# Kernel tuning notes

Hardware: AMD Instinct MI355X
Metric: run time of the kernel (lower is better)

Reference implementation:

```python
import jax, jax.numpy as jnp
import numpy as np

N_NODES = 50000
IN_F = 512
OUT_F = 512
N_EDGES = 1600000
DROP_P = 0.5
NEG_SLOPE = 0.01  # torch LeakyReLU default


def leaky_relu(x):
    return jnp.where(x >= 0, x, NEG_SLOPE * x)


def setup_inputs() -> dict:
    key = jax.random.key(0)
    k1, k2, k3, k4, k5, k6 = jax.random.split(key, 6)
    x = jax.random.normal(k1, (N_NODES, IN_F), dtype=jnp.float32)
    W = jax.random.normal(k2, (OUT_F, IN_F), dtype=jnp.float32) * (1.0 / np.sqrt(IN_F))
    # inverted dropout mask: bernoulli(keep)/keep, keep = 1 - p
    keep = 1.0 - DROP_P
    drop_mask = (jax.random.uniform(k3, (N_NODES, IN_F)) < keep).astype(jnp.float32) / keep
    adj_vals = jax.random.uniform(k4, (N_EDGES,), dtype=jnp.float32)
    adj_rows = jax.random.randint(k5, (N_EDGES,), 0, N_NODES, dtype=jnp.int32)
    adj_cols = jax.random.randint(k6, (N_EDGES,), 0, N_NODES, dtype=jnp.int32)
    return {"x": x, "W": W, "drop_mask": drop_mask, "adj_vals": adj_vals,
            "adj_rows": adj_rows, "adj_cols": adj_cols}


def reference(x, W, drop_mask, adj_vals, adj_rows, adj_cols):
    # support = Linear(dropout(x)); Linear weight is [out, in] (torch convention)
    support = jnp.einsum('ni,oi->no', x * drop_mask, W)  # [N, out]
    h = leaky_relu(support)
    # sparse adj @ h: out[r] += v * h[c]
    msgs = adj_vals[:, None] * h[adj_cols]               # [E, out]
    agg = jax.ops.segment_sum(msgs, adj_rows, num_segments=N_NODES)
    return leaky_relu(agg)
```

## Files before the change

### kernel.cpp

```cpp
#include <hip/hip_runtime.h>

#define NROWS 50000
#define NFEAT 512
#define NEDGE 1600000
#define SLOPE 0.01f

typedef unsigned short u16;
typedef __attribute__((ext_vector_type(8))) short short8;
typedef __attribute__((ext_vector_type(4))) float f32x4;
typedef __attribute__((ext_vector_type(4))) int i32x4;
typedef __attribute__((ext_vector_type(2))) unsigned uintx2;
typedef __attribute__((ext_vector_type(8))) unsigned short u16x8;

__device__ __forceinline__ u16 f2bf(float f) {
  unsigned u = __float_as_uint(f);
  u += 0x7fffu + ((u >> 16) & 1u);
  return (u16)(u >> 16);
}
__device__ __forceinline__ float lrelu(float v) { return v >= 0.f ? v : SLOPE * v; }

__global__ void prep_kernel(const float* __restrict__ w, u16* __restrict__ wb,
                            const int* __restrict__ rows, int* __restrict__ counts) {
  const int stride = gridDim.x * blockDim.x;
  const int tid0 = blockIdx.x * blockDim.x + threadIdx.x;
  for (int i = tid0; i < (NFEAT * NFEAT) / 8; i += stride) {
    size_t b = (size_t)i * 2;
    f32x4 a0 = __builtin_nontemporal_load(&((const f32x4*)w)[b]);
    f32x4 a1 = __builtin_nontemporal_load(&((const f32x4*)w)[b + 1]);
    u16x8 o;
    o[0] = f2bf(a0[0]); o[1] = f2bf(a0[1]); o[2] = f2bf(a0[2]); o[3] = f2bf(a0[3]);
    o[4] = f2bf(a1[0]); o[5] = f2bf(a1[1]); o[6] = f2bf(a1[2]); o[7] = f2bf(a1[3]);
    *(u16x8*)(wb + (size_t)i * 8) = o;
  }
  for (int i = tid0; i < NEDGE / 4; i += stride) {
    i32x4 r4 = __builtin_nontemporal_load(&((const i32x4*)rows)[i]);
    atomicAdd(&counts[r4[0]], 1);
    atomicAdd(&counts[r4[1]], 1);
    atomicAdd(&counts[r4[2]], 1);
    atomicAdd(&counts[r4[3]], 1);
  }
}

__global__ void scan_kernel(const int* __restrict__ counts, int* __restrict__ offs) {
  __shared__ int wpre[17];
  const int t = threadIdx.x;
  const int lane = t & 63, w = t >> 6;
  const int beg = t * 64;
  i32x4 c4[16];
  int s = 0;
  if (beg < NROWS) {
#pragma unroll
    for (int g = 0; g < 16; ++g) {
      int idx = beg + g * 4;
      if (idx < NROWS) {
        c4[g] = ((const i32x4*)counts)[idx >> 2];
        s += c4[g][0] + c4[g][1] + c4[g][2] + c4[g][3];
      }
    }
  }
  int inc = s;
#pragma unroll
  for (int d = 1; d < 64; d <<= 1) {
    int u = __shfl_up(inc, d);
    if (lane >= d) inc += u;
  }
  if (lane == 63) wpre[w + 1] = inc;
  __syncthreads();
  if (t == 0) {
    wpre[0] = 0;
    for (int i = 1; i <= 16; ++i) wpre[i] += wpre[i - 1];
    offs[NROWS] = wpre[16];
  }
  __syncthreads();
  int run = wpre[w] + inc - s;
  if (beg < NROWS) {
#pragma unroll
    for (int g = 0; g < 16; ++g) {
      int idx = beg + g * 4;
      if (idx < NROWS) {
        i32x4 o;
        o[0] = run; run += c4[g][0];
        o[1] = run; run += c4[g][1];
        o[2] = run; run += c4[g][2];
        o[3] = run; run += c4[g][3];
        ((i32x4*)offs)[idx >> 2] = o;
      }
    }
  }
}

__global__ void scatter_kernel(const float* __restrict__ vals, const int* __restrict__ rows,
                               const int* __restrict__ cols, const int* __restrict__ offs,
                               int* __restrict__ cursor, unsigned* __restrict__ svc) {
  int e0 = (blockIdx.x * blockDim.x + threadIdx.x) * 4;
  if (e0 >= NEDGE) return;
  i32x4 r4 = __builtin_nontemporal_load((const i32x4*)(rows + e0));
  i32x4 c4 = __builtin_nontemporal_load((const i32x4*)(cols + e0));
  f32x4 v4 = __builtin_nontemporal_load((const f32x4*)(vals + e0));
#pragma unroll
  for (int j = 0; j < 4; ++j) {
    int p = offs[r4[j]] + atomicAdd(&cursor[r4[j]], 1);
    svc[p] = ((unsigned)c4[j] << 16) | (unsigned)f2bf(v4[j]);
  }
}

__global__ __launch_bounds__(512) void gemm_kernel(const float* __restrict__ x,
                                                   const float* __restrict__ msk,
                                                   const u16* __restrict__ wb,
                                                   unsigned char* __restrict__ hq,
                                                   float* __restrict__ scaleg) {
  __shared__ __align__(16) char smem[64 * 512];
  __shared__ float wmax[8][64];
  __shared__ float rinv4[4][64];
  u16* lA = (u16*)smem;
  const int tid = threadIdx.x;
  const int lane = tid & 63;
  const int wv = tid >> 6;
  const long rowBase = (long)blockIdx.x * 64;

  f32x4 acc[4][4] = {};

  const int srow = tid >> 3;
  const int sk8 = tid & 7;
  const int swslot = (sk8 ^ (srow & 7)) * 8;
  long sgr = rowBase + srow;
  if (sgr > NROWS - 1) sgr = NROWS - 1;
  const float* xp = x + sgr * 512 + sk8 * 8;
  const float* mp = msk + sgr * 512 + sk8 * 8;
  u16* swr = lA + srow * 64 + swslot;

  const int rsel = lane & 15, kgrp = (lane >> 4) * 8;
  const u16* bbase = wb + ((long)(wv * 64 + rsel)) * 512 + kgrp;

  for (int k0 = 0; k0 < 512; k0 += 64) {
    f32x4 xa = __builtin_nontemporal_load((const f32x4*)(xp + k0));
    f32x4 xb = __builtin_nontemporal_load((const f32x4*)(xp + k0 + 4));
    f32x4 ma = __builtin_nontemporal_load((const f32x4*)(mp + k0));
    f32x4 mb = __builtin_nontemporal_load((const f32x4*)(mp + k0 + 4));
    short8 b[4][2];
#pragma unroll
    for (int n = 0; n < 4; ++n) {
#pragma unroll
      for (int kk = 0; kk < 2; ++kk)
        b[n][kk] = *(const short8*)(bbase + (long)n * 16 * 512 + k0 + kk * 32);
    }
    __syncthreads();
    u16x8 o;
    o[0] = f2bf(xa[0] * ma[0]); o[1] = f2bf(xa[1] * ma[1]);
    o[2] = f2bf(xa[2] * ma[2]); o[3] = f2bf(xa[3] * ma[3]);
    o[4] = f2bf(xb[0] * mb[0]); o[5] = f2bf(xb[1] * mb[1]);
    o[6] = f2bf(xb[2] * mb[2]); o[7] = f2bf(xb[3] * mb[3]);
    *(u16x8*)swr = o;
    __syncthreads();
    short8 a[4][2];
#pragma unroll
    for (int m = 0; m < 4; ++m) {
      int ar = m * 16 + rsel;
      const u16* base = lA + ar * 64;
      int sw = (ar & 7) << 3;
      a[m][0] = *(const short8*)(base + (kgrp ^ sw));
      a[m][1] = *(const short8*)(base + ((32 + kgrp) ^ sw));
    }
#pragma unroll
    for (int kk = 0; kk < 2; ++kk)
#pragma unroll
      for (int m = 0; m < 4; ++m)
#pragma unroll
        for (int n = 0; n < 4; ++n)
          acc[m][n] = __builtin_amdgcn_mfma_f32_16x16x32_bf16(a[m][kk], b[n][kk], acc[m][n], 0, 0, 0);
  }

  const int crow = (lane >> 4) * 4;
  const int ccol = lane & 15;

  float pm[4][4];
#pragma unroll
  for (int m = 0; m < 4; ++m)
#pragma unroll
    for (int r2 = 0; r2 < 4; ++r2) {
      float mx = 0.f;
#pragma unroll
      for (int n = 0; n < 4; ++n) mx = fmaxf(mx, fabsf(lrelu(acc[m][n][r2])));
      pm[m][r2] = mx;
    }
#pragma unroll
  for (int d = 1; d < 16; d <<= 1)
#pragma unroll
    for (int m = 0; m < 4; ++m)
#pragma unroll
      for (int r2 = 0; r2 < 4; ++r2) pm[m][r2] = fmaxf(pm[m][r2], __shfl_xor(pm[m][r2], d));
  if ((lane & 15) == 0) {
#pragma unroll
    for (int m = 0; m < 4; ++m)
#pragma unroll
      for (int r2 = 0; r2 < 4; ++r2) wmax[wv][m * 16 + crow + r2] = pm[m][r2];
  }
  __syncthreads();
  if (tid < 256) {
    int g = tid >> 6, row = tid & 63;
    float rm = fmaxf(wmax[2 * g][row], wmax[2 * g + 1][row]);
    float s = rm > 0.f ? rm * (1.f / 127.f) : 1.f;
    rinv4[g][row] = rm > 0.f ? 127.f / rm : 0.f;
    long gr = rowBase + row;
    if (gr < NROWS) scaleg[gr * 4 + g] = s;
  }
  __syncthreads();

  unsigned char* lT = (unsigned char*)smem;
  const int qg = wv >> 1;
#pragma unroll
  for (int m = 0; m < 4; ++m) {
    int row0 = m * 16 + crow;
    float ri0 = rinv4[qg][row0], ri1 = rinv4[qg][row0 + 1];
    float ri2 = rinv4[qg][row0 + 2], ri3 = rinv4[qg][row0 + 3];
#pragma unroll
    for (int n = 0; n < 4; ++n) {
      int col = wv * 64 + n * 16 + ccol;
      int cg = col & 127;
      float q0 = rintf(lrelu(acc[m][n][0]) * ri0);
      float q1 = rintf(lrelu(acc[m][n][1]) * ri1);
      float q2 = rintf(lrelu(acc[m][n][2]) * ri2);
      float q3 = rintf(lrelu(acc[m][n][3]) * ri3);
      int i0 = min(127, max(-127, (int)q0));
      int i1 = min(127, max(-127, (int)q1));
      int i2 = min(127, max(-127, (int)q2));
      int i3 = min(127, max(-127, (int)q3));
      unsigned pk = (i0 & 0xff) | ((i1 & 0xff) << 8) | ((i2 & 0xff) << 16) | ((i3 & 0xff) << 24);
#pragma unroll
      for (int r2 = 0; r2 < 4; ++r2) {
        int row = row0 + r2;
        lT[row * 512 + (qg << 7) + (cg ^ ((row & 7) << 4))] = (unsigned char)(pk >> (8 * r2));
      }
    }
  }
  __syncthreads();
  {
    const int row = tid >> 3, seg = tid & 7;
    long gr = rowBase + row;
    if (gr < NROWS) {
      unsigned char* dst = hq + gr * 512;
#pragma unroll
      for (int j = 0; j < 4; ++j) {
        int gc = seg * 4 + j;
        int g2 = gc >> 3, s = gc & 7;
        i32x4 vv = *(const i32x4*)(lT + row * 512 + g2 * 128 + ((s ^ (row & 7)) << 4));
        *(i32x4*)(dst + gc * 16) = vv;
      }
    }
  }
}

__global__ __launch_bounds__(256) void aggregate_kernel(const unsigned char* __restrict__ hq,
                                                        const float* __restrict__ scaleg,
                                                        const unsigned* __restrict__ svc,
                                                        const int* __restrict__ offs,
                                                        float* __restrict__ out) {
  const int lane = threadIdx.x & 63;
  const int wid = threadIdx.x >> 6;
  const int r = blockIdx.x * 4 + wid;
  if (r >= NROWS) return;
  const int beg = offs[r], end = offs[r + 1];
  const int half = lane >> 5, sub = lane & 31;
  const int grp = sub >> 3;
  float a[16] = {};
  const unsigned char* hp = hq + sub * 16;
  unsigned cb[4], nb[4];
  const int n = end - beg;
  const int ng = n >> 3;
  if (ng > 0) {
#pragma unroll
    for (int k = 0; k < 4; ++k) cb[k] = svc[beg + 2 * k + half];
  }
  for (int g = 0; g < ng; ++g) {
    if (g + 1 < ng) {
#pragma unroll
      for (int k = 0; k < 4; ++k) nb[k] = svc[beg + (g + 1) * 8 + 2 * k + half];
    }
#pragma unroll
    for (int k = 0; k < 4; ++k) {
      float v = __uint_as_float(cb[k] << 16);
      size_t c = (size_t)(cb[k] >> 16);
      float vs = v * scaleg[c * 4 + grp];
      i32x4 q = *(const i32x4*)(hp + c * 512);
#pragma unroll
      for (int j = 0; j < 4; ++j) {
        unsigned qq = (unsigned)q[j];
        a[4 * j + 0] += vs * (float)(signed char)(qq);
        a[4 * j + 1] += vs * (float)(signed char)(qq >> 8);
        a[4 * j + 2] += vs * (float)(signed char)(qq >> 16);
        a[4 * j + 3] += vs * (float)(signed char)(qq >> 24);
      }
    }
    if (g + 1 < ng) {
#pragma unroll
      for (int k = 0; k < 4; ++k) cb[k] = nb[k];
    }
  }
  int e = beg + ng * 8;
  for (; e + 1 < end; e += 2) {
    unsigned u = svc[e + half];
    float v = __uint_as_float(u << 16);
    size_t c = (size_t)(u >> 16);
    float vs = v * scaleg[c * 4 + grp];
    i32x4 q = *(const i32x4*)(hp + c * 512);
#pragma unroll
    for (int j = 0; j < 4; ++j) {
      unsigned qq = (unsigned)q[j];
      a[4 * j + 0] += vs * (float)(signed char)(qq);
      a[4 * j + 1] += vs * (float)(signed char)(qq >> 8);
      a[4 * j + 2] += vs * (float)(signed char)(qq >> 16);
      a[4 * j + 3] += vs * (float)(signed char)(qq >> 24);
    }
  }
  if (e < end) {
    unsigned u = svc[e];
    float v = __uint_as_float(u << 16);
    size_t c = (size_t)(u >> 16);
    float vs = half ? 0.f : v * scaleg[c * 4 + grp];
    i32x4 q = *(const i32x4*)(hp + c * 512);
#pragma unroll
    for (int j = 0; j < 4; ++j) {
      unsigned qq = (unsigned)q[j];
      a[4 * j + 0] += vs * (float)(signed char)(qq);
      a[4 * j + 1] += vs * (float)(signed char)(qq >> 8);
      a[4 * j + 2] += vs * (float)(signed char)(qq >> 16);
      a[4 * j + 3] += vs * (float)(signed char)(qq >> 24);
    }
  }
#pragma unroll
  for (int j = 0; j < 16; ++j) a[j] += __shfl_xor(a[j], 32);
  if (half == 0) {
    float* op = out + (size_t)r * NFEAT + sub * 16;
#pragma unroll
    for (int j = 0; j < 4; ++j) {
      f32x4 o;
      o[0] = lrelu(a[4 * j + 0]);
      o[1] = lrelu(a[4 * j + 1]);
      o[2] = lrelu(a[4 * j + 2]);
      o[3] = lrelu(a[4 * j + 3]);
      *(f32x4*)(op + 4 * j) = o;
    }
  }
}

extern "C" void kernel_launch(void* const* d_in, const int* in_sizes, int n_in,
                              void* d_out, int out_size, void* d_ws, size_t ws_size,
                              hipStream_t stream) {
  const float* x = (const float*)d_in[0];
  const float* W = (const float*)d_in[1];
  const float* mask = (const float*)d_in[2];
  const float* vals = (const float*)d_in[3];
  const int* rows = (const int*)d_in[4];
  const int* cols = (const int*)d_in[5];
  float* out = (float*)d_out;
  char* ws = (char*)d_ws;

  const size_t o_hq = 0;
  const size_t o_wb = o_hq + 25600000;
  const size_t o_scale = o_wb + 524288;
  const size_t o_counts = o_scale + 800000;
  const size_t o_cursor = o_counts + 200000;
  const size_t o_offs = o_cursor + 200000;
  const size_t o_svc = o_offs + 200064;

  unsigned char* hq = (unsigned char*)(ws + o_hq);
  u16* wb = (u16*)(ws + o_wb);
  float* scaleg = (float*)(ws + o_scale);
  int* counts = (int*)(ws + o_counts);
  int* cursor = (int*)(ws + o_cursor);
  int* offs = (int*)(ws + o_offs);
  unsigned* svc = (unsigned*)(ws + o_svc);

  hipMemsetAsync(counts, 0, 400000, stream);

  prep_kernel<<<1024, 256, 0, stream>>>(W, wb, rows, counts);
  scan_kernel<<<1, 1024, 0, stream>>>(counts, offs);
  scatter_kernel<<<1563, 256, 0, stream>>>(vals, rows, cols, offs, cursor, svc);
  gemm_kernel<<<782, 512, 0, stream>>>(x, mask, wb, hq, scaleg);
  aggregate_kernel<<<12500, 256, 0, stream>>>(hq, scaleg, svc, offs, out);
}
```

Before: 421.4 us.

## Double-buffer A tile in LDS and prefetch next x/mask tile in GEMM

The GEMM main loop now uses two LDS buffers for the bf16 A tile. Each iteration prefetches the x/mask data two steps ahead and writes the next tile while the current one is consumed, which cuts the loop to one barrier. The goal is to hide global load latency of x and mask behind the MFMA work. In exchange it holds more registers for the prefetched values and fully unrolls the loop.

```diff
diff --git a/kernel.cpp b/kernel.cpp
--- a/kernel.cpp
+++ b/kernel.cpp
@@ -9,7 +9,6 @@
 typedef __attribute__((ext_vector_type(8))) short short8;
 typedef __attribute__((ext_vector_type(4))) float f32x4;
 typedef __attribute__((ext_vector_type(4))) int i32x4;
-typedef __attribute__((ext_vector_type(2))) unsigned uintx2;
 typedef __attribute__((ext_vector_type(8))) unsigned short u16x8;
 
 __device__ __forceinline__ u16 f2bf(float f) {
@@ -112,7 +111,8 @@
   __shared__ __align__(16) char smem[64 * 512];
   __shared__ float wmax[8][64];
   __shared__ float rinv4[4][64];
-  u16* lA = (u16*)smem;
+  u16* lA0 = (u16*)smem;
+  u16* lA1 = (u16*)(smem + 8192);
   const int tid = threadIdx.x;
   const int lane = tid & 63;
   const int wv = tid >> 6;
@@ -122,21 +122,41 @@
 
   const int srow = tid >> 3;
   const int sk8 = tid & 7;
-  const int swslot = (sk8 ^ (srow & 7)) * 8;
+  const int swoff = srow * 64 + (sk8 ^ (srow & 7)) * 8;
   long sgr = rowBase + srow;
   if (sgr > NROWS - 1) sgr = NROWS - 1;
   const float* xp = x + sgr * 512 + sk8 * 8;
   const float* mp = msk + sgr * 512 + sk8 * 8;
-  u16* swr = lA + srow * 64 + swslot;
 
   const int rsel = lane & 15, kgrp = (lane >> 4) * 8;
   const u16* bbase = wb + ((long)(wv * 64 + rsel)) * 512 + kgrp;
 
-  for (int k0 = 0; k0 < 512; k0 += 64) {
-    f32x4 xa = __builtin_nontemporal_load((const f32x4*)(xp + k0));
-    f32x4 xb = __builtin_nontemporal_load((const f32x4*)(xp + k0 + 4));
-    f32x4 ma = __builtin_nontemporal_load((const f32x4*)(mp + k0));
-    f32x4 mb = __builtin_nontemporal_load((const f32x4*)(mp + k0 + 4));
+  f32x4 xa, xb, ma, mb;
+#define LOADT(K)                                                   \
+  xa = __builtin_nontemporal_load((const f32x4*)(xp + (K)));       \
+  xb = __builtin_nontemporal_load((const f32x4*)(xp + (K) + 4));   \
+  ma = __builtin_nontemporal_load((const f32x4*)(mp + (K)));       \
+  mb = __builtin_nontemporal_load((const f32x4*)(mp + (K) + 4));
+#define WRITET(BUF)                                                \
+  {                                                                \
+    u16x8 o;                                                       \
+    o[0] = f2bf(xa[0] * ma[0]); o[1] = f2bf(xa[1] * ma[1]);        \
+    o[2] = f2bf(xa[2] * ma[2]); o[3] = f2bf(xa[3] * ma[3]);        \
+    o[4] = f2bf(xb[0] * mb[0]); o[5] = f2bf(xb[1] * mb[1]);        \
+    o[6] = f2bf(xb[2] * mb[2]); o[7] = f2bf(xb[3] * mb[3]);        \
+    *(u16x8*)((BUF) + swoff) = o;                                  \
+  }
+
+  LOADT(0);
+  WRITET(lA0);
+  LOADT(64);
+
+#pragma unroll
+  for (int t = 0; t < 8; ++t) {
+    const int k0 = t * 64;
+    u16* cur = (t & 1) ? lA1 : lA0;
+    u16* nxt = (t & 1) ? lA0 : lA1;
+    __syncthreads();
     short8 b[4][2];
 #pragma unroll
     for (int n = 0; n < 4; ++n) {
@@ -144,23 +164,19 @@
       for (int kk = 0; kk < 2; ++kk)
         b[n][kk] = *(const short8*)(bbase + (long)n * 16 * 512 + k0 + kk * 32);
     }
-    __syncthreads();
-    u16x8 o;
-    o[0] = f2bf(xa[0] * ma[0]); o[1] = f2bf(xa[1] * ma[1]);
-    o[2] = f2bf(xa[2] * ma[2]); o[3] = f2bf(xa[3] * ma[3]);
-    o[4] = f2bf(xb[0] * mb[0]); o[5] = f2bf(xb[1] * mb[1]);
-    o[6] = f2bf(xb[2] * mb[2]); o[7] = f2bf(xb[3] * mb[3]);
-    *(u16x8*)swr = o;
-    __syncthreads();
     short8 a[4][2];
 #pragma unroll
     for (int m = 0; m < 4; ++m) {
       int ar = m * 16 + rsel;
-      const u16* base = lA + ar * 64;
+      const u16* base = cur + ar * 64;
       int sw = (ar & 7) << 3;
       a[m][0] = *(const short8*)(base + (kgrp ^ sw));
       a[m][1] = *(const short8*)(base + ((32 + kgrp) ^ sw));
     }
+    if (t < 7) {
+      WRITET(nxt);
+      if (t < 6) { LOADT(k0 + 128); }
+    }
 #pragma unroll
     for (int kk = 0; kk < 2; ++kk)
 #pragma unroll
@@ -169,6 +185,8 @@
         for (int n = 0; n < 4; ++n)
           acc[m][n] = __builtin_amdgcn_mfma_f32_16x16x32_bf16(a[m][kk], b[n][kk], acc[m][n], 0, 0, 0);
   }
+#undef LOADT
+#undef WRITET
 
   const int crow = (lane >> 4) * 4;
   const int ccol = lane & 15;
```

After: 416.1 us. About the same (-1.2%).
